# Optimization experiments

Hardware: AMD Instinct MI355X
Metric: run time of the kernel (lower is better)

The kernel has to match this reference:

```python
import jax, jax.numpy as jnp
import numpy as np

LM_DIM = 4096
V_DIM = 1024
N_V = 32
FF = 1024
IN_DIM = V_DIM * N_V + LM_DIM  # 36864
B = 16
T = 2048


def setup_inputs() -> dict:
    key = jax.random.key(0)
    ks = jax.random.split(key, 16)
    grd_hidden = jax.random.normal(ks[0], (T, LM_DIM), dtype=jnp.float32)
    vision_features = jax.random.normal(ks[1], (B, N_V, V_DIM), dtype=jnp.float32)
    token_batch_idx = jnp.sort(jax.random.randint(ks[2], (T,), 0, B, dtype=jnp.int64))
    def lin(k, fan_in, fan_out):
        kw, kb = jax.random.split(k)
        scale = jnp.sqrt(2.0 / (fan_in + fan_out)).astype(jnp.float32)
        W = jax.random.normal(kw, (fan_in, fan_out), dtype=jnp.float32) * scale
        b = jnp.zeros((fan_out,), dtype=jnp.float32)
        return W, b
    W1, b1 = lin(ks[3], IN_DIM, FF)
    W2, b2 = lin(ks[4], FF, FF)
    W3, b3 = lin(ks[5], FF, FF)
    W4, b4 = lin(ks[6], FF, FF)
    W5, b5 = lin(ks[7], FF, 6)
    return {"grd_hidden": grd_hidden, "vision_features": vision_features,
            "token_batch_idx": token_batch_idx,
            "W1": W1, "b1": b1, "W2": W2, "b2": b2, "W3": W3, "b3": b3,
            "W4": W4, "b4": b4, "W5": W5, "b5": b5}


def reference(grd_hidden, vision_features, token_batch_idx,
              W1, b1, W2, b2, W3, b3, W4, b4, W5, b5):
    # flatten vision latents per sample: [B, N_V*V_DIM]
    vis_flat = vision_features.reshape(vision_features.shape[0], -1)
    # per-token gather of the sample's vision feature: [T, N_V*V_DIM]
    vis_per_tok = vis_flat[token_batch_idx]
    # concat(vision, language) per token, then shared 5-layer MLP
    x = jnp.concatenate([vis_per_tok, grd_hidden], axis=-1)  # [T, IN_DIM]
    h = jax.nn.relu(x @ W1 + b1)
    h = jax.nn.relu(h @ W2 + b2)
    h = jax.nn.relu(h @ W3 + b3)
    h = jax.nn.relu(h @ W4 + b4)
    return h @ W5 + b5  # [T, 6]
```

## Files before the change

kernel.cpp:

```cpp
#include <hip/hip_runtime.h>


typedef __attribute__((ext_vector_type(8))) short bf16x8;
typedef __attribute__((ext_vector_type(4))) float f32x4;

#define LM_DIM 4096
#define V_DIM  1024
#define N_V    32
#define FF     1024
#define VIS_K  (V_DIM * N_V)
#define NB     16
#define NTOK   2048

__device__ __forceinline__ unsigned short f2bf(float f) {
    unsigned int u = __float_as_uint(f);
    u += 0x7fffu + ((u >> 16) & 1u);
    return (unsigned short)(u >> 16);
}
__device__ __forceinline__ float bf2f(unsigned short s) {
    return __uint_as_float(((unsigned int)s) << 16);
}

__device__ __forceinline__ void gload_lds16(const void* g, void* lds) {
    __builtin_amdgcn_global_load_lds(
        (const __attribute__((address_space(1))) unsigned int*)g,
        (__attribute__((address_space(3))) unsigned int*)lds,
        16, 0, 0);
}

__global__ void zero_vc(float* __restrict__ vc) {
    int i = blockIdx.x * blockDim.x + threadIdx.x;
    vc[i] = 0.f;
}

__global__ __launch_bounds__(1024) void vis_contrib(
    const float* __restrict__ W1, const float* __restrict__ vis,
    float* __restrict__ vc)
{
    const int n  = threadIdx.x;
    const int k0 = blockIdx.x * 128;
    __shared__ float sv[NB][128];
    for (int idx = threadIdx.x; idx < NB * 128; idx += 1024) {
        int b = idx >> 7, kk = idx & 127;
        sv[b][kk] = vis[(size_t)b * VIS_K + k0 + kk];
    }
    __syncthreads();
    float acc[NB];
#pragma unroll
    for (int b = 0; b < NB; ++b) acc[b] = 0.f;
    for (int kk = 0; kk < 128; ++kk) {
        float w = W1[(size_t)(k0 + kk) * FF + n];
#pragma unroll
        for (int b = 0; b < NB; ++b) acc[b] += sv[b][kk] * w;
    }
#pragma unroll
    for (int b = 0; b < NB; ++b) atomicAdd(&vc[b * FF + n], acc[b]);
}

__global__ void cvt_f32_bf16(const float* __restrict__ in,
                             unsigned short* __restrict__ out, int n8) {
    int i = blockIdx.x * blockDim.x + threadIdx.x;
    if (i >= n8) return;
    const float4* p = (const float4*)in + (size_t)i * 2;
    float4 a = p[0], b = p[1];
    union { unsigned short us[8]; uint4 v; } o;
    o.us[0] = f2bf(a.x); o.us[1] = f2bf(a.y); o.us[2] = f2bf(a.z); o.us[3] = f2bf(a.w);
    o.us[4] = f2bf(b.x); o.us[5] = f2bf(b.y); o.us[6] = f2bf(b.z); o.us[7] = f2bf(b.w);
    ((uint4*)out)[i] = o.v;
}

__global__ void tr_cvt(const float* __restrict__ src,
                       unsigned short* __restrict__ dst, int K, int N) {
    __shared__ float t[64][65];
    const int k0 = blockIdx.x * 64, n0 = blockIdx.y * 64;
    const int tx = threadIdx.x, ty = threadIdx.y;
    for (int r = ty; r < 64; r += 4)
        t[r][tx] = src[(size_t)(k0 + r) * N + n0 + tx];
    __syncthreads();
    for (int r = ty; r < 64; r += 4)
        dst[(size_t)(n0 + r) * K + k0 + tx] = f2bf(t[tx][r]);
}

template <int EPI>
__global__ __launch_bounds__(256, 2) void gemm_bt(
    const unsigned short* __restrict__ A,
    const unsigned short* __restrict__ BT,
    const float* __restrict__ bias,
    const float* __restrict__ Vc,
    const int* __restrict__ tbi,
    unsigned short* __restrict__ Hout,
    int M, int N, int K)
{
    __shared__ __align__(16) unsigned char smem[16384];
    unsigned char* sA = smem;
    unsigned char* sB = smem + 8192;

    const int tid  = threadIdx.x;
    const int lane = tid & 63;
    const int wv   = tid >> 6;
    const int wr   = wv >> 1;
    const int wc   = wv & 1;
    const int bm   = blockIdx.x * 64;
    const int bn   = blockIdx.y * 64;

    f32x4 acc[2][2];
#pragma unroll
    for (int m = 0; m < 2; ++m)
#pragma unroll
        for (int n = 0; n < 2; ++n) acc[m][n] = (f32x4){0.f, 0.f, 0.f, 0.f};

    for (int k0 = 0; k0 < K; k0 += 64) {
        __syncthreads();
#pragma unroll
        for (int c = 0; c < 2; ++c) {
            int seg = wv * 2 + c;
            int p   = seg * 1024 + lane * 16;
            int row = p >> 7;
            int kb  = (p & 127) ^ ((row & 7) << 4);
            gload_lds16((const unsigned char*)A + ((size_t)(bm + row) * K + k0) * 2 + kb,
                        sA + seg * 1024);
        }
#pragma unroll
        for (int c = 0; c < 2; ++c) {
            int seg = wv * 2 + c;
            int p   = seg * 1024 + lane * 16;
            int row = p >> 7;
            int kb  = (p & 127) ^ ((row & 7) << 4);
            gload_lds16((const unsigned char*)BT + ((size_t)(bn + row) * K + k0) * 2 + kb,
                        sB + seg * 1024);
        }
        __syncthreads();

#pragma unroll
        for (int kk = 0; kk < 2; ++kk) {
            const int kbb = kk * 64 + (lane >> 4) * 16;
            bf16x8 av[2], bv[2];
#pragma unroll
            for (int m = 0; m < 2; ++m) {
                int r = wr * 32 + m * 16 + (lane & 15);
                av[m] = *(const bf16x8*)(sA + r * 128 + (kbb ^ ((r & 7) << 4)));
            }
#pragma unroll
            for (int n = 0; n < 2; ++n) {
                int r = wc * 32 + n * 16 + (lane & 15);
                bv[n] = *(const bf16x8*)(sB + r * 128 + (kbb ^ ((r & 7) << 4)));
            }
#pragma unroll
            for (int m = 0; m < 2; ++m)
#pragma unroll
                for (int n = 0; n < 2; ++n)
                    acc[m][n] = __builtin_amdgcn_mfma_f32_16x16x32_bf16(
                        av[m], bv[n], acc[m][n], 0, 0, 0);
        }
    }

#pragma unroll
    for (int m = 0; m < 2; ++m) {
#pragma unroll
        for (int j = 0; j < 4; ++j) {
            int grow = bm + wr * 32 + m * 16 + (lane >> 4) * 4 + j;
            const float* vrow = (EPI == 1) ? (Vc + (size_t)tbi[grow] * N) : nullptr;
#pragma unroll
            for (int n = 0; n < 2; ++n) {
                int gcol = bn + wc * 32 + n * 16 + (lane & 15);
                float v = acc[m][n][j] + bias[gcol];
                if (EPI == 1) v += vrow[gcol];
                v = fmaxf(v, 0.f);
                Hout[(size_t)grow * N + gcol] = f2bf(v);
            }
        }
    }
}

__global__ __launch_bounds__(256) void final_proj(
    const unsigned short* __restrict__ H, const float* __restrict__ W5,
    const float* __restrict__ b5, float* __restrict__ out)
{
    const int t    = blockIdx.x * 4 + (threadIdx.x >> 6);
    const int lane = threadIdx.x & 63;
    float s[6] = {0.f, 0.f, 0.f, 0.f, 0.f, 0.f};
#pragma unroll
    for (int i = 0; i < 16; ++i) {
        int k = i * 64 + lane;
        float h = bf2f(H[(size_t)t * FF + k]);
#pragma unroll
        for (int j = 0; j < 6; ++j) s[j] += h * W5[(size_t)k * 6 + j];
    }
#pragma unroll
    for (int j = 0; j < 6; ++j) {
#pragma unroll
        for (int off = 32; off > 0; off >>= 1) s[j] += __shfl_down(s[j], off);
    }
    if (lane == 0) {
#pragma unroll
        for (int j = 0; j < 6; ++j) out[(size_t)t * 6 + j] = s[j] + b5[j];
    }
}

extern "C" void kernel_launch(void* const* d_in, const int* in_sizes, int n_in,
                              void* d_out, int out_size, void* d_ws, size_t ws_size,
                              hipStream_t stream) {
    const float* grd = (const float*)d_in[0];
    const float* vis = (const float*)d_in[1];
    const int*   tbi = (const int*)d_in[2];
    const float* W1  = (const float*)d_in[3];
    const float* b1  = (const float*)d_in[4];
    const float* W2  = (const float*)d_in[5];
    const float* b2  = (const float*)d_in[6];
    const float* W3  = (const float*)d_in[7];
    const float* b3  = (const float*)d_in[8];
    const float* W4  = (const float*)d_in[9];
    const float* b4  = (const float*)d_in[10];
    const float* W5  = (const float*)d_in[11];
    const float* b5  = (const float*)d_in[12];
    float* out = (float*)d_out;

    char* ws = (char*)d_ws;
    float*          Vc    = (float*)ws;
    unsigned short* grdb  = (unsigned short*)(ws + (1u << 16));
    unsigned short* W1lT  = (unsigned short*)(ws + 16842752);
    unsigned short* W2T   = (unsigned short*)(ws + 25231360);
    unsigned short* W3T   = (unsigned short*)(ws + 27328512);
    unsigned short* W4T   = (unsigned short*)(ws + 29425664);
    unsigned short* hA    = (unsigned short*)(ws + 31522816);
    unsigned short* hB    = (unsigned short*)(ws + 35717120);

    zero_vc<<<16, 1024, 0, stream>>>(Vc);
    vis_contrib<<<256, 1024, 0, stream>>>(W1, vis, Vc);

    cvt_f32_bf16<<<4096, 256, 0, stream>>>(grd, grdb, NTOK * LM_DIM / 8);
    tr_cvt<<<dim3(LM_DIM / 64, FF / 64), dim3(64, 4), 0, stream>>>(
        W1 + (size_t)VIS_K * FF, W1lT, LM_DIM, FF);
    tr_cvt<<<dim3(FF / 64, FF / 64), dim3(64, 4), 0, stream>>>(W2, W2T, FF, FF);
    tr_cvt<<<dim3(FF / 64, FF / 64), dim3(64, 4), 0, stream>>>(W3, W3T, FF, FF);
    tr_cvt<<<dim3(FF / 64, FF / 64), dim3(64, 4), 0, stream>>>(W4, W4T, FF, FF);

    gemm_bt<1><<<dim3(NTOK / 64, FF / 64), 256, 0, stream>>>(
        grdb, W1lT, b1, Vc, tbi, hA, NTOK, FF, LM_DIM);
    gemm_bt<0><<<dim3(NTOK / 64, FF / 64), 256, 0, stream>>>(
        hA, W2T, b2, nullptr, nullptr, hB, NTOK, FF, FF);
    gemm_bt<0><<<dim3(NTOK / 64, FF / 64), 256, 0, stream>>>(
        hB, W3T, b3, nullptr, nullptr, hA, NTOK, FF, FF);
    gemm_bt<0><<<dim3(NTOK / 64, FF / 64), 256, 0, stream>>>(
        hA, W4T, b4, nullptr, nullptr, hB, NTOK, FF, FF);
    final_proj<<<NTOK / 4, 256, 0, stream>>>(hB, W5, b5, out);
}
```

Baseline: 383.9 us.

## Double-buffer GEMM LDS, swizzle block order, fuse prep kernels, replace atomics with partial reduce

The GEMM kernel now double-buffers its LDS tiles, issuing the next k-tile's global-to-LDS loads before computing the current one, with one barrier per iteration. Workgroup ids are remapped in strides of eight, presumably to spread neighbouring tiles across XCDs. The conversion and transpose kernels are merged into one launch to cut launch overhead. The vision contribution now writes per-slice partial sums that a second kernel reduces, so far fewer atomics are issued. The cost is 16 MB of extra workspace traffic for the partials and twice the LDS per GEMM block, which may lower occupancy.

Result: faster. 356.6 us (-7.1%).

```diff
diff --git a/kernel.cpp b/kernel.cpp
--- a/kernel.cpp
+++ b/kernel.cpp
@@ -5,10 +5,8 @@
 typedef __attribute__((ext_vector_type(4))) float f32x4;
 
 #define LM_DIM 4096
-#define V_DIM  1024
-#define N_V    32
 #define FF     1024
-#define VIS_K  (V_DIM * N_V)
+#define VIS_K  32768
 #define NB     16
 #define NTOK   2048
 
@@ -28,17 +26,13 @@
         16, 0, 0);
 }
 
-__global__ void zero_vc(float* __restrict__ vc) {
-    int i = blockIdx.x * blockDim.x + threadIdx.x;
-    vc[i] = 0.f;
-}
-
-__global__ __launch_bounds__(1024) void vis_contrib(
+__global__ __launch_bounds__(1024) void vis_partial(
     const float* __restrict__ W1, const float* __restrict__ vis,
-    float* __restrict__ vc)
+    float* __restrict__ pb)
 {
     const int n  = threadIdx.x;
-    const int k0 = blockIdx.x * 128;
+    const int ks = blockIdx.x;
+    const int k0 = ks * 128;
     __shared__ float sv[NB][128];
     for (int idx = threadIdx.x; idx < NB * 128; idx += 1024) {
         int b = idx >> 7, kk = idx & 127;
@@ -54,28 +48,59 @@
         for (int b = 0; b < NB; ++b) acc[b] += sv[b][kk] * w;
     }
 #pragma unroll
-    for (int b = 0; b < NB; ++b) atomicAdd(&vc[b * FF + n], acc[b]);
-}
-
-__global__ void cvt_f32_bf16(const float* __restrict__ in,
-                             unsigned short* __restrict__ out, int n8) {
-    int i = blockIdx.x * blockDim.x + threadIdx.x;
-    if (i >= n8) return;
-    const float4* p = (const float4*)in + (size_t)i * 2;
-    float4 a = p[0], b = p[1];
-    union { unsigned short us[8]; uint4 v; } o;
-    o.us[0] = f2bf(a.x); o.us[1] = f2bf(a.y); o.us[2] = f2bf(a.z); o.us[3] = f2bf(a.w);
-    o.us[4] = f2bf(b.x); o.us[5] = f2bf(b.y); o.us[6] = f2bf(b.z); o.us[7] = f2bf(b.w);
-    ((uint4*)out)[i] = o.v;
-}
-
-__global__ void tr_cvt(const float* __restrict__ src,
-                       unsigned short* __restrict__ dst, int K, int N) {
+    for (int b = 0; b < NB; ++b)
+        pb[((size_t)ks * NB + b) * FF + n] = acc[b];
+}
+
+__global__ __launch_bounds__(256) void vis_reduce(
+    const float* __restrict__ pb, float* __restrict__ vc)
+{
+    const int lin = blockIdx.x * 256 + threadIdx.x;
+    const int n = lin & 1023;
+    const int r = lin >> 10;
+    const int b = r >> 2;
+    const int q = r & 3;
+    float s = 0.f;
+#pragma unroll 4
+    for (int i = 0; i < 64; ++i) {
+        int ks = q * 64 + i;
+        s += pb[((size_t)ks * NB + b) * FF + n];
+    }
+    atomicAdd(&vc[b * FF + n], s);
+}
+
+__global__ __launch_bounds__(256) void prep_all(
+    const float* __restrict__ grd, unsigned short* __restrict__ grdb,
+    const float* __restrict__ W1l, unsigned short* __restrict__ W1lT,
+    const float* __restrict__ W2,  unsigned short* __restrict__ W2T,
+    const float* __restrict__ W3,  unsigned short* __restrict__ W3T,
+    const float* __restrict__ W4,  unsigned short* __restrict__ W4T)
+{
     __shared__ float t[64][65];
-    const int k0 = blockIdx.x * 64, n0 = blockIdx.y * 64;
+    const int bid = blockIdx.x;
     const int tx = threadIdx.x, ty = threadIdx.y;
+
+    if (bid < 4096) {
+        int i = bid * 256 + ty * 64 + tx;
+        const float4* p = (const float4*)grd + (size_t)i * 2;
+        float4 a = p[0], bvec = p[1];
+        union { unsigned short us[8]; uint4 v; } o;
+        o.us[0] = f2bf(a.x); o.us[1] = f2bf(a.y);
+        o.us[2] = f2bf(a.z); o.us[3] = f2bf(a.w);
+        o.us[4] = f2bf(bvec.x); o.us[5] = f2bf(bvec.y);
+        o.us[6] = f2bf(bvec.z); o.us[7] = f2bf(bvec.w);
+        ((uint4*)grdb)[i] = o.v;
+        return;
+    }
+    const float* src; unsigned short* dst; int K, tt;
+    if (bid < 5120)      { src = W1l; dst = W1lT; K = LM_DIM; tt = bid - 4096; }
+    else if (bid < 5376) { src = W2;  dst = W2T;  K = FF;     tt = bid - 5120; }
+    else if (bid < 5632) { src = W3;  dst = W3T;  K = FF;     tt = bid - 5376; }
+    else                 { src = W4;  dst = W4T;  K = FF;     tt = bid - 5632; }
+    const int tilesx = K / 64;
+    const int k0 = (tt % tilesx) * 64, n0 = (tt / tilesx) * 64;
     for (int r = ty; r < 64; r += 4)
-        t[r][tx] = src[(size_t)(k0 + r) * N + n0 + tx];
+        t[r][tx] = src[(size_t)(k0 + r) * FF + n0 + tx];
     __syncthreads();
     for (int r = ty; r < 64; r += 4)
         dst[(size_t)(n0 + r) * K + k0 + tx] = f2bf(t[tx][r]);
@@ -91,46 +116,46 @@
     unsigned short* __restrict__ Hout,
     int M, int N, int K)
 {
-    __shared__ __align__(16) unsigned char smem[16384];
-    unsigned char* sA = smem;
-    unsigned char* sB = smem + 8192;
+    __shared__ __align__(16) unsigned char smem[32768];
 
     const int tid  = threadIdx.x;
     const int lane = tid & 63;
     const int wv   = tid >> 6;
     const int wr   = wv >> 1;
     const int wc   = wv & 1;
-    const int bm   = blockIdx.x * 64;
-    const int bn   = blockIdx.y * 64;
-
+
+    const int nwg  = gridDim.x * gridDim.y;
+    const int bid0 = blockIdx.y * gridDim.x + blockIdx.x;
+    const int cpx  = nwg >> 3;
+    const int bid  = (bid0 & 7) * cpx + (bid0 >> 3);
+    const int bm   = (bid % gridDim.x) * 64;
+    const int bn   = (bid / gridDim.x) * 64;
+
+    const int seg  = wv * 2;
     f32x4 acc[2][2];
 #pragma unroll
     for (int m = 0; m < 2; ++m)
 #pragma unroll
         for (int n = 0; n < 2; ++n) acc[m][n] = (f32x4){0.f, 0.f, 0.f, 0.f};
 
-    for (int k0 = 0; k0 < K; k0 += 64) {
-        __syncthreads();
+    auto stage = [&](int p, int k0) {
+        unsigned char* sA = smem + p * 16384;
+        unsigned char* sB = sA + 8192;
 #pragma unroll
         for (int c = 0; c < 2; ++c) {
-            int seg = wv * 2 + c;
-            int p   = seg * 1024 + lane * 16;
-            int row = p >> 7;
-            int kb  = (p & 127) ^ ((row & 7) << 4);
-            gload_lds16((const unsigned char*)A + ((size_t)(bm + row) * K + k0) * 2 + kb,
-                        sA + seg * 1024);
+            int sg  = seg + c;
+            int off = sg * 1024 + lane * 16;
+            int row = off >> 7;
+            int kb  = (off & 127) ^ ((row & 7) << 4);
+            gload_lds16((const unsigned char*)A  + ((size_t)(bm + row) * K + k0) * 2 + kb,
+                        sA + sg * 1024);
+            gload_lds16((const unsigned char*)BT + ((size_t)(bn + row) * K + k0) * 2 + kb,
+                        sB + sg * 1024);
         }
-#pragma unroll
-        for (int c = 0; c < 2; ++c) {
-            int seg = wv * 2 + c;
-            int p   = seg * 1024 + lane * 16;
-            int row = p >> 7;
-            int kb  = (p & 127) ^ ((row & 7) << 4);
-            gload_lds16((const unsigned char*)BT + ((size_t)(bn + row) * K + k0) * 2 + kb,
-                        sB + seg * 1024);
-        }
-        __syncthreads();
-
+    };
+    auto compute = [&](int p) {
+        const unsigned char* sA = smem + p * 16384;
+        const unsigned char* sB = sA + 8192;
 #pragma unroll
         for (int kk = 0; kk < 2; ++kk) {
             const int kbb = kk * 64 + (lane >> 4) * 16;
@@ -152,6 +177,15 @@
                     acc[m][n] = __builtin_amdgcn_mfma_f32_16x16x32_bf16(
                         av[m], bv[n], acc[m][n], 0, 0, 0);
         }
+    };
+
+    const int nt = K >> 6;
+    stage(0, 0);
+    __syncthreads();
+    for (int t = 0; t < nt; ++t) {
+        if (t + 1 < nt) stage((t + 1) & 1, (t + 1) << 6);
+        compute(t & 1);
+        __syncthreads();
     }
 
 #pragma unroll
@@ -216,24 +250,22 @@
     float* out = (float*)d_out;
 
     char* ws = (char*)d_ws;
-    float*          Vc    = (float*)ws;
-    unsigned short* grdb  = (unsigned short*)(ws + (1u << 16));
-    unsigned short* W1lT  = (unsigned short*)(ws + 16842752);
-    unsigned short* W2T   = (unsigned short*)(ws + 25231360);
-    unsigned short* W3T   = (unsigned short*)(ws + 27328512);
-    unsigned short* W4T   = (unsigned short*)(ws + 29425664);
-    unsigned short* hA    = (unsigned short*)(ws + 31522816);
-    unsigned short* hB    = (unsigned short*)(ws + 35717120);
-
-    zero_vc<<<16, 1024, 0, stream>>>(Vc);
-    vis_contrib<<<256, 1024, 0, stream>>>(W1, vis, Vc);
-
-    cvt_f32_bf16<<<4096, 256, 0, stream>>>(grd, grdb, NTOK * LM_DIM / 8);
-    tr_cvt<<<dim3(LM_DIM / 64, FF / 64), dim3(64, 4), 0, stream>>>(
-        W1 + (size_t)VIS_K * FF, W1lT, LM_DIM, FF);
-    tr_cvt<<<dim3(FF / 64, FF / 64), dim3(64, 4), 0, stream>>>(W2, W2T, FF, FF);
-    tr_cvt<<<dim3(FF / 64, FF / 64), dim3(64, 4), 0, stream>>>(W3, W3T, FF, FF);
-    tr_cvt<<<dim3(FF / 64, FF / 64), dim3(64, 4), 0, stream>>>(W4, W4T, FF, FF);
+    float*          pb    = (float*)ws;
+    float*          Vc    = (float*)(ws + 16777216);
+    unsigned short* grdb  = (unsigned short*)(ws + 16842752);
+    unsigned short* W1lT  = (unsigned short*)(ws + 33619968);
+    unsigned short* W2T   = (unsigned short*)(ws + 42008576);
+    unsigned short* W3T   = (unsigned short*)(ws + 44105728);
+    unsigned short* W4T   = (unsigned short*)(ws + 46202880);
+    unsigned short* hA    = (unsigned short*)(ws + 48300032);
+    unsigned short* hB    = (unsigned short*)(ws + 52494336);
+
+    hipMemsetAsync(Vc, 0, NB * FF * sizeof(float), stream);
+    vis_partial<<<256, 1024, 0, stream>>>(W1, vis, pb);
+    vis_reduce<<<256, 256, 0, stream>>>(pb, Vc);
+
+    prep_all<<<5888, dim3(64, 4), 0, stream>>>(
+        grd, grdb, W1 + (size_t)VIS_K * FF, W1lT, W2, W2T, W3, W3T, W4, W4T);
 
     gemm_bt<1><<<dim3(NTOK / 64, FF / 64), 256, 0, stream>>>(
         grdb, W1lT, b1, Vc, tbi, hA, NTOK, FF, LM_DIM);
@@ -243,5 +275,6 @@
         hB, W3T, b3, nullptr, nullptr, hA, NTOK, FF, FF);
     gemm_bt<0><<<dim3(NTOK / 64, FF / 64), 256, 0, stream>>>(
         hA, W4T, b4, nullptr, nullptr, hB, NTOK, FF, FF);
+
     final_proj<<<NTOK / 4, 256, 0, stream>>>(hB, W5, b5, out);
 }
```
